# Performance work log

Measured on AMD Instinct MI355X. Metric: run time of the kernel, lower is better.

The kernel has to match this reference:

```python
import jax, jax.numpy as jnp
import numpy as np
import math

B, T, V, D, H, L = 32, 512, 16, 256, 4, 2

def _ln(x, g, b, eps=1e-5):
    m = jnp.mean(x, -1, keepdims=True)
    v = jnp.mean((x - m) ** 2, -1, keepdims=True)
    return (x - m) * jax.lax.rsqrt(v + eps) * g + b

def _grn(x, w1, b1, w2, b2, g, bn, sw=None, sb=None):
    h = jax.nn.elu(x @ w1 + b1)
    h = h @ w2 + b2
    h1, h2 = jnp.split(h, 2, axis=-1)
    h = h1 * jax.nn.sigmoid(h2)
    skip = x if sw is None else x @ sw + sb
    return _ln(h + skip, g, bn)

def setup_inputs():
    ks = iter(jax.random.split(jax.random.key(0), 64))
    s = 0.02
    def w(*shape):
        return jax.random.normal(next(ks), shape, jnp.float32) * s
    return dict(
        x=jax.random.normal(next(ks), (B, T, V), jnp.float32),
        emb_w=w(V, D), emb_b=w(V, D),
        vg_fc1_w=w(V, D, D), vg_fc1_b=w(V, D), vg_fc2_w=w(V, D, 2 * D), vg_fc2_b=w(V, 2 * D),
        vg_ln_g=jnp.ones((V, D), jnp.float32), vg_ln_b=jnp.zeros((V, D), jnp.float32),
        sel_fc1_w=w(V * D, D), sel_fc1_b=w(D), sel_fc2_w=w(D, 2 * V), sel_fc2_b=w(2 * V),
        sel_skip_w=w(V * D, V), sel_skip_b=w(V),
        sel_ln_g=jnp.ones((V,), jnp.float32), sel_ln_b=jnp.zeros((V,), jnp.float32),
        lstm_wih=w(L, 4 * D, D), lstm_whh=w(L, 4 * D, D), lstm_bih=w(L, 4 * D), lstm_bhh=w(L, 4 * D),
        pl_fc1_w=w(D, D), pl_fc1_b=w(D), pl_fc2_w=w(D, 2 * D), pl_fc2_b=w(2 * D),
        pl_ln_g=jnp.ones((D,), jnp.float32), pl_ln_b=jnp.zeros((D,), jnp.float32),
        attn_in_w=w(3 * D, D), attn_in_b=w(3 * D), attn_out_w=w(D, D), attn_out_b=w(D),
        attn_ln_g=jnp.ones((D,), jnp.float32), attn_ln_b=jnp.zeros((D,), jnp.float32),
        pa_fc1_w=w(D, D), pa_fc1_b=w(D), pa_fc2_w=w(D, 2 * D), pa_fc2_b=w(2 * D),
        pa_ln_g=jnp.ones((D,), jnp.float32), pa_ln_b=jnp.zeros((D,), jnp.float32),
        fg_fc1_w=w(D, 4 * D), fg_fc1_b=w(4 * D), fg_fc2_w=w(4 * D, 2 * D), fg_fc2_b=w(2 * D),
        fg_ln_g=jnp.ones((D,), jnp.float32), fg_ln_b=jnp.zeros((D,), jnp.float32),
    )

def reference(x, emb_w, emb_b, vg_fc1_w, vg_fc1_b, vg_fc2_w, vg_fc2_b, vg_ln_g, vg_ln_b,
              sel_fc1_w, sel_fc1_b, sel_fc2_w, sel_fc2_b, sel_skip_w, sel_skip_b, sel_ln_g, sel_ln_b,
              lstm_wih, lstm_whh, lstm_bih, lstm_bhh,
              pl_fc1_w, pl_fc1_b, pl_fc2_w, pl_fc2_b, pl_ln_g, pl_ln_b,
              attn_in_w, attn_in_b, attn_out_w, attn_out_b, attn_ln_g, attn_ln_b,
              pa_fc1_w, pa_fc1_b, pa_fc2_w, pa_fc2_b, pa_ln_g, pa_ln_b,
              fg_fc1_w, fg_fc1_b, fg_fc2_w, fg_fc2_b, fg_ln_g, fg_ln_b):
    b, t, v = x.shape
    d = emb_w.shape[1]
    # per-feature Linear(1, d) fused into one broadcasted op: [B,T,V,D]
    embedded = x[..., None] * emb_w + emb_b
    # per-variable GRNs (no skip_fc since input==output), batched over V via einsum
    h = jax.nn.elu(jnp.einsum('btvd,vdh->btvh', embedded, vg_fc1_w) + vg_fc1_b)
    h = jnp.einsum('btvh,vho->btvo', h, vg_fc2_w) + vg_fc2_b
    h1, h2 = jnp.split(h, 2, axis=-1)
    var_out = _ln(h1 * jax.nn.sigmoid(h2) + embedded, vg_ln_g, vg_ln_b)  # [B,T,V,D]
    # selection GRN over flattened variables
    flat = embedded.reshape(b, t, v * d)
    sel = _grn(flat, sel_fc1_w, sel_fc1_b, sel_fc2_w, sel_fc2_b, sel_ln_g, sel_ln_b, sel_skip_w, sel_skip_b)
    weights = jax.nn.softmax(sel, axis=-1)  # [B,T,V]
    vsn_out = jnp.einsum('btvh,btv->bth', var_out, weights)  # [B,T,D]
    # stacked LSTM (torch gate order i,f,g,o); dropout inactive at eval
    h_seq = vsn_out
    for l in range(lstm_wih.shape[0]):
        xi = jnp.einsum('btd,gd->btg', h_seq, lstm_wih[l]) + lstm_bih[l] + lstm_bhh[l]
        whh = lstm_whh[l]
        def step(carry, xt):
            hp, cp = carry
            gates = xt + hp @ whh.T
            i, f, g, o = jnp.split(gates, 4, axis=-1)
            c = jax.nn.sigmoid(f) * cp + jax.nn.sigmoid(i) * jnp.tanh(g)
            hh = jax.nn.sigmoid(o) * jnp.tanh(c)
            return (hh, c), hh
        init = (jnp.zeros((b, d), x.dtype), jnp.zeros((b, d), x.dtype))
        _, hs = jax.lax.scan(step, init, jnp.swapaxes(xi, 0, 1))
        h_seq = jnp.swapaxes(hs, 0, 1)
    lstm_filtered = _grn(h_seq + vsn_out, pl_fc1_w, pl_fc1_b, pl_fc2_w, pl_fc2_b, pl_ln_g, pl_ln_b)
    # multihead self-attention
    qkv = lstm_filtered @ attn_in_w.T + attn_in_b
    q, k, vv = jnp.split(qkv, 3, axis=-1)
    hd = d // H
    def heads(z):
        return z.reshape(b, t, H, hd).transpose(0, 2, 1, 3)
    q, k, vv = heads(q), heads(k), heads(vv)
    scale = 1.0 / math.sqrt(hd)
    att = jax.nn.softmax(jnp.einsum('bhqd,bhkd->bhqk', q, k) * scale, axis=-1)
    o = jnp.einsum('bhqk,bhkd->bhqd', att, vv).transpose(0, 2, 1, 3).reshape(b, t, d)
    o = o @ attn_out_w.T + attn_out_b
    attn_out = _ln(o + lstm_filtered, attn_ln_g, attn_ln_b)
    attn_filtered = _grn(attn_out, pa_fc1_w, pa_fc1_b, pa_fc2_w, pa_fc2_b, pa_ln_g, pa_ln_b)
    out = _grn(attn_filtered, fg_fc1_w, fg_fc1_b, fg_fc2_w, fg_fc2_b, fg_ln_g, fg_ln_b)
    return out[:, -1, :], weights
```

## Files before the change

### kernel.cpp

```cpp
#include <hip/hip_runtime.h>
#include <hip/hip_bf16.h>
#include <hip/hip_fp8.h>
#include <math.h>


#define BT 16384
#define TT 512
#define BB 32
#define VV 16
#define DD 256

typedef unsigned short ushort;
typedef unsigned int uint;
typedef unsigned long ulong_;
typedef __attribute__((ext_vector_type(8))) short short8;
typedef __attribute__((ext_vector_type(8))) unsigned short ushort8v;
typedef __attribute__((ext_vector_type(4))) float floatx4;
typedef __attribute__((ext_vector_type(8))) int int8v;

#if __has_builtin(__builtin_amdgcn_cvt_pk_fp8_f32)
#define HW_FP8_CVT 1
#endif

__device__ __forceinline__ float sigmoidf_(float x) { return 1.f / (1.f + expf(-x)); }
__device__ __forceinline__ float eluf_(float x)     { return x > 0.f ? x : expm1f(x); }
__device__ __forceinline__ float fsig(float x) {
  return __builtin_amdgcn_rcpf(1.f + __expf(-x));
}
__device__ __forceinline__ float ftanh(float x) {
  float xc = fminf(fmaxf(x, -44.f), 44.f);
  float e = __expf(-2.f * xc);
  return (1.f - e) * __builtin_amdgcn_rcpf(1.f + e);
}
__device__ __forceinline__ ushort f2bf(float f) {
  unsigned int u = __float_as_uint(f);
  unsigned int r = u + 0x7fffu + ((u >> 16) & 1u);
  return (ushort)(r >> 16);
}
__device__ __forceinline__ float bf2f(ushort b) { return __uint_as_float(((unsigned int)b) << 16); }

__device__ __forceinline__ float bsum256(float v, float* red4) {
  #pragma unroll
  for (int m = 32; m > 0; m >>= 1) v += __shfl_xor(v, m, 64);
  int w = threadIdx.x >> 6;
  if ((threadIdx.x & 63) == 0) red4[w] = v;
  __syncthreads();
  float r = red4[0] + red4[1] + red4[2] + red4[3];
  __syncthreads();
  return r;
}

__device__ __forceinline__ float block_sum256(float v, float* red) {
  int j = threadIdx.x;
  red[j] = v; __syncthreads();
  #pragma unroll
  for (int st = 128; st > 0; st >>= 1) {
    if (j < st) red[j] += red[j + st];
    __syncthreads();
  }
  float r = red[0];
  __syncthreads();
  return r;
}

__global__ void wtT_k(const float* __restrict__ src, ushort* __restrict__ dst,
                      int K, int N, long sStride, long dStride) {
  int b = blockIdx.z;
  src += (size_t)b * sStride; dst += (size_t)b * dStride;
  __shared__ float t[32][33];
  int k0 = blockIdx.y * 32, n0 = blockIdx.x * 32;
  int tx = threadIdx.x & 31, ty = threadIdx.x >> 5;
  #pragma unroll
  for (int i = 0; i < 32; i += 8) {
    int k = k0 + ty + i, n = n0 + tx;
    t[ty + i][tx] = (k < K && n < N) ? src[(size_t)k * N + n] : 0.f;
  }
  __syncthreads();
  #pragma unroll
  for (int i = 0; i < 32; i += 8) {
    int n = n0 + ty + i, k = k0 + tx;
    if (n < N && k < K) dst[(size_t)n * K + k] = f2bf(t[tx][ty + i]);
  }
}

__global__ void cvt_k(const float* __restrict__ src, ushort* __restrict__ dst, int n) {
  int i = blockIdx.x * 256 + threadIdx.x;
  if (i < n) dst[i] = f2bf(src[i]);
}

__global__ void whh_pack8_k(const float* __restrict__ whh, unsigned char* __restrict__ dst) {
  int gid = blockIdx.x * 256 + threadIdx.x;
  int layer = gid >> 13;
  int rem = gid & 8191;
  int lane = rem & 63;
  int f = (rem >> 6) & 15;
  int wave = rem >> 10;
  int kt2 = f & 1, ts = (f >> 1) & 1, g = f >> 2;
  int n = g * 256 + wave * 32 + ts * 16 + (lane & 15);
  int k0 = kt2 * 128 + (lane >> 4) * 32;
  const float* src = whh + (size_t)layer * 262144 + (size_t)n * 256 + k0;
  unsigned char* d = dst + (size_t)gid * 32;
  #pragma unroll
  for (int b = 0; b < 32; b++) {
    __hip_fp8_e4m3 q(src[b] * 64.f);
    d[b] = q.__x;
  }
}

template<int ADT, int ACT, int CDT>
__global__ __launch_bounds__(256) void mgemm_k(
    const void* __restrict__ Aall, int lda, long aStride,
    const ushort* __restrict__ Ball, long bStride,
    const float* __restrict__ biasAll, long biasStride,
    void* __restrict__ Call, int ldc, long cStride,
    int K, int Nvalid,
    const float* __restrict__ embw, const float* __restrict__ embb, int xbase) {
  int z = blockIdx.z;
  const ushort* B = Ball + (size_t)z * bStride;
  const float* bias = biasAll ? biasAll + (size_t)z * biasStride : nullptr;
  int m0 = blockIdx.y * 128, n0 = blockIdx.x * 128;
  __shared__ ushort As[128][40];
  __shared__ ushort Bs[128][40];
  int tid = threadIdx.x;
  int r = tid >> 1, half = tid & 1;
  int wave = tid >> 6, lane = tid & 63;
  int wm = (wave >> 1) * 64, wn = (wave & 1) * 64;
  int lm = lane & 15, lq = lane >> 4;
  floatx4 acc[4][4];
  #pragma unroll
  for (int i = 0; i < 4; i++)
    #pragma unroll
    for (int j = 0; j < 4; j++) acc[i][j] = (floatx4)0.f;

  for (int k0 = 0; k0 < K; k0 += 32) {
    int kk = k0 + half * 16;
    {
      int gm = m0 + r;
      ushort tmp[16];
      if (ADT == 0) {
        const float* Af = (const float*)Aall + (size_t)z * aStride + (size_t)gm * lda + kk;
        #pragma unroll
        for (int q = 0; q < 4; q++) {
          float4 f = ((const float4*)Af)[q];
          tmp[q * 4 + 0] = f2bf(f.x); tmp[q * 4 + 1] = f2bf(f.y);
          tmp[q * 4 + 2] = f2bf(f.z); tmp[q * 4 + 3] = f2bf(f.w);
        }
      } else if (ADT == 1) {
        const ushort* Ab = (const ushort*)Aall + (size_t)z * aStride + (size_t)gm * lda + kk;
        *(ushort8v*)&tmp[0] = *(const ushort8v*)(Ab);
        *(ushort8v*)&tmp[8] = *(const ushort8v*)(Ab + 8);
      } else {
        const float* xp = (const float*)Aall;
        float xv = xp[(size_t)gm * lda + xbase + z + (kk >> 8)];
        const float4* ew = (const float4*)(embw + (size_t)z * 256 + kk);
        const float4* eb = (const float4*)(embb + (size_t)z * 256 + kk);
        #pragma unroll
        for (int q = 0; q < 4; q++) {
          float4 w4 = ew[q], b4 = eb[q];
          tmp[q * 4 + 0] = f2bf(xv * w4.x + b4.x); tmp[q * 4 + 1] = f2bf(xv * w4.y + b4.y);
          tmp[q * 4 + 2] = f2bf(xv * w4.z + b4.z); tmp[q * 4 + 3] = f2bf(xv * w4.w + b4.w);
        }
      }
      *(ushort8v*)&As[r][half * 16]     = *(ushort8v*)&tmp[0];
      *(ushort8v*)&As[r][half * 16 + 8] = *(ushort8v*)&tmp[8];
    }
    {
      int gn = n0 + r;
      ushort tmp[16];
      if (gn < Nvalid) {
        const ushort* Bp = B + (size_t)gn * K + kk;
        *(ushort8v*)&tmp[0] = *(const ushort8v*)(Bp);
        *(ushort8v*)&tmp[8] = *(const ushort8v*)(Bp + 8);
      } else {
        #pragma unroll
        for (int q = 0; q < 16; q++) tmp[q] = 0;
      }
      *(ushort8v*)&Bs[r][half * 16]     = *(ushort8v*)&tmp[0];
      *(ushort8v*)&Bs[r][half * 16 + 8] = *(ushort8v*)&tmp[8];
    }
    __syncthreads();
    short8 fa[4], fb[4];
    #pragma unroll
    for (int i = 0; i < 4; i++) fa[i] = *(const short8*)&As[wm + i * 16 + lm][lq * 8];
    #pragma unroll
    for (int j = 0; j < 4; j++) fb[j] = *(const short8*)&Bs[wn + j * 16 + lm][lq * 8];
    #pragma unroll
    for (int i = 0; i < 4; i++)
      #pragma unroll
      for (int j = 0; j < 4; j++)
        acc[i][j] = __builtin_amdgcn_mfma_f32_16x16x32_bf16(fa[i], fb[j], acc[i][j], 0, 0, 0);
    __syncthreads();
  }
  #pragma unroll
  for (int j = 0; j < 4; j++) {
    int gn = n0 + wn + j * 16 + lm;
    if (gn >= Nvalid) continue;
    float bv = bias ? bias[gn] : 0.f;
    #pragma unroll
    for (int i = 0; i < 4; i++) {
      #pragma unroll
      for (int rg = 0; rg < 4; rg++) {
        int gm = m0 + wm + i * 16 + lq * 4 + rg;
        float v = acc[i][j][rg] + bv;
        if (ACT == 1) v = eluf_(v);
        if (CDT == 0) ((float*)Call + (size_t)z * cStride)[(size_t)gm * ldc + gn] = v;
        else ((ushort*)Call + (size_t)z * cStride)[(size_t)gm * ldc + gn] = f2bf(v);
      }
    }
  }
}

__global__ void sel_finish_k(const float* __restrict__ selG, const float* __restrict__ selSkip,
                             const float* __restrict__ lng, const float* __restrict__ lnb,
                             float* __restrict__ wout, int M) {
  int m = blockIdx.x * 256 + threadIdx.x;
  if (m >= M) return;
  float s[16];
  float mean = 0.f;
  #pragma unroll
  for (int i = 0; i < 16; i++) {
    float h1 = selG[m * 32 + i], h2 = selG[m * 32 + 16 + i];
    float val = h1 * sigmoidf_(h2) + selSkip[m * 16 + i];
    s[i] = val; mean += val;
  }
  mean *= (1.f / 16.f);
  float var = 0.f;
  #pragma unroll
  for (int i = 0; i < 16; i++) { float d = s[i] - mean; var += d * d; }
  var *= (1.f / 16.f);
  float inv = rsqrtf(var + 1e-5f);
  float mx = -1e30f;
  #pragma unroll
  for (int i = 0; i < 16; i++) { s[i] = (s[i] - mean) * inv * lng[i] + lnb[i]; mx = fmaxf(mx, s[i]); }
  float sum = 0.f;
  #pragma unroll
  for (int i = 0; i < 16; i++) { s[i] = expf(s[i] - mx); sum += s[i]; }
  float isum = 1.f / sum;
  #pragma unroll
  for (int i = 0; i < 16; i++) wout[m * 16 + i] = s[i] * isum;
}

__global__ __launch_bounds__(256) void var_epi4_k(
    const ushort* __restrict__ G16,
    const float* __restrict__ x, int vbase,
    const float* __restrict__ embw, const float* __restrict__ embb,
    const float* __restrict__ lng, const float* __restrict__ lnb,
    const float* __restrict__ wts, float* __restrict__ vsn, int first) {
  int m = blockIdx.x, j = threadIdx.x;
  __shared__ float red4[4];
  float accv = 0.f;
  #pragma unroll
  for (int z = 0; z < 4; z++) {
    int v = vbase + z;
    const ushort* Gp = G16 + ((size_t)z * BT + m) * 512;
    float g1 = bf2f(Gp[j]), g2 = bf2f(Gp[256 + j]);
    float e = x[m * VV + v] * embw[z * 256 + j] + embb[z * 256 + j];
    float s = g1 * sigmoidf_(g2) + e;
    float mean = bsum256(s, red4) * (1.f / 256.f);
    float d = s - mean;
    float var = bsum256(d * d, red4) * (1.f / 256.f);
    float o = d * rsqrtf(var + 1e-5f) * lng[z * 256 + j] + lnb[z * 256 + j];
    accv += wts[m * VV + v] * o;
  }
  size_t oi = (size_t)m * 256 + j;
  if (first) vsn[oi] = accv; else vsn[oi] += accv;
}

__global__ __launch_bounds__(256) void grn_epi_k(
    const ushort* __restrict__ G, const float* __restrict__ skip,
    const float* __restrict__ lng, const float* __restrict__ lnb,
    float* __restrict__ out) {
  int m = blockIdx.x, j = threadIdx.x;
  __shared__ float red4[4];
  float g1 = bf2f(G[(size_t)m * 512 + j]), g2 = bf2f(G[(size_t)m * 512 + 256 + j]);
  float s = g1 * sigmoidf_(g2) + skip[(size_t)m * 256 + j];
  float mean = bsum256(s, red4) * (1.f / 256.f);
  float d = s - mean;
  float var = bsum256(d * d, red4) * (1.f / 256.f);
  out[(size_t)m * 256 + j] = d * rsqrtf(var + 1e-5f) * lng[j] + lnb[j];
}

__global__ void add2_k(const float* __restrict__ a, const float* __restrict__ b,
                       float* __restrict__ c, int n) {
  int i = blockIdx.x * 256 + threadIdx.x;
  if (i < n) c[i] = a[i] + b[i];
}

#define DESC (1.f / 1024.f)
#define H8S 272
__global__ __launch_bounds__(512, 2) void lstm_recur_k(
    const float* __restrict__ xi,
    const unsigned char* __restrict__ wpk,
    float* __restrict__ hout,
    int T) {
  int bb = blockIdx.x;
  int tid = threadIdx.x;
  int wave = tid >> 6, lane = tid & 63;
  int lm = lane & 15, lq = lane >> 4;
  __shared__ __align__(16) unsigned char h8[2][16 * H8S];
  for (int i = tid; i < 2 * 16 * H8S / 4; i += 512) ((uint*)h8)[i] = 0;

  int8v wr[16];
  {
    const int8v* wp = (const int8v*)wpk;
    #pragma unroll
    for (int f = 0; f < 16; f++) wr[f] = wp[(wave * 16 + f) * 64 + lane];
  }
  bool act = (lq == 0);
  int jj = wave * 32 + lm;
  const float* xg = xi + (size_t)bb * T * 1024;
  float xq[8], xn[8];
  if (act) {
    #pragma unroll
    for (int g = 0; g < 4; g++) {
      xq[2 * g]     = xg[g * 256 + jj];
      xq[2 * g + 1] = xg[g * 256 + jj + 16];
    }
  }
  float cst[2] = {0.f, 0.f};
  float hbf[2][8];
  int arow = lm * H8S + lq * 32;
  __syncthreads();

  for (int t = 0; t < T; t++) {
    int cur = t & 1, nxt = cur ^ 1;
    if (act && t + 1 < T) {
      const float* xp = xg + (size_t)(t + 1) * 1024;
      #pragma unroll
      for (int g = 0; g < 4; g++) {
        xn[2 * g]     = xp[g * 256 + jj];
        xn[2 * g + 1] = xp[g * 256 + jj + 16];
      }
    }
    int8v a[2];
    #pragma unroll
    for (int kt = 0; kt < 2; kt++)
      a[kt] = *(const int8v*)&h8[cur][arow + kt * 128];
    floatx4 acc[8];
    #pragma unroll
    for (int f = 0; f < 8; f++) acc[f] = (floatx4)0.f;
    #pragma unroll
    for (int kt = 0; kt < 2; kt++)
      #pragma unroll
      for (int f = 0; f < 8; f++)
        acc[f] = __builtin_amdgcn_mfma_scale_f32_16x16x128_f8f6f4(
            a[kt], wr[f * 2 + kt], acc[f], 0, 0, 0, 0x7f7f7f7f, 0, 0x7f7f7f7f);
    if (act) {
      int tb = t & 7;
      #pragma unroll
      for (int ts = 0; ts < 2; ts++) {
        float pi = acc[0 + ts][0] * DESC + xq[0 + ts];
        float pf = acc[2 + ts][0] * DESC + xq[2 + ts];
        float pg = acc[4 + ts][0] * DESC + xq[4 + ts];
        float po = acc[6 + ts][0] * DESC + xq[6 + ts];
        float c = fsig(pf) * cst[ts] + fsig(pi) * ftanh(pg);
        cst[ts] = c;
        hbf[ts][tb] = fsig(po) * ftanh(c);
      }
#ifdef HW_FP8_CVT
      int pk = __builtin_amdgcn_cvt_pk_fp8_f32(hbf[0][tb] * 16.f, hbf[1][tb] * 16.f, 0, false);
      h8[nxt][jj]      = (unsigned char)(pk & 0xff);
      h8[nxt][jj + 16] = (unsigned char)((pk >> 8) & 0xff);
#else
      __hip_fp8_e4m3 q0(hbf[0][tb] * 16.f), q1(hbf[1][tb] * 16.f);
      h8[nxt][jj]      = q0.__x;
      h8[nxt][jj + 16] = q1.__x;
#endif
      if (tb == 7) {
        #pragma unroll
        for (int q = 0; q < 8; q++) {
          size_t base = ((size_t)(bb * T + t - 7 + q)) * 256;
          hout[base + jj]      = hbf[0][q];
          hout[base + jj + 16] = hbf[1][q];
        }
      }
      #pragma unroll
      for (int g = 0; g < 8; g++) xq[g] = xn[g];
    }
    __syncthreads();
  }
}

__global__ __launch_bounds__(256) void attn_decode_k(const float* __restrict__ qkv,
                                                     float* __restrict__ o, int T) {
  int bh = blockIdx.x; int b = bh >> 2, h = bh & 3;
  int tid = threadIdx.x;
  __shared__ float q[64];
  __shared__ float p[512];
  __shared__ float red[256];
  if (tid < 64) q[tid] = qkv[((size_t)(b * T + T - 1)) * 768 + h * 64 + tid];
  __syncthreads();
  for (int t = tid; t < 512; t += 256) {
    const float* kv = qkv + ((size_t)(b * T + t)) * 768 + 256 + h * 64;
    float s = 0.f;
    #pragma unroll 16
    for (int d = 0; d < 64; d++) s += q[d] * kv[d];
    p[t] = s * 0.125f;
  }
  __syncthreads();
  red[tid] = fmaxf(p[tid], p[tid + 256]); __syncthreads();
  for (int st = 128; st > 0; st >>= 1) { if (tid < st) red[tid] = fmaxf(red[tid], red[tid + st]); __syncthreads(); }
  float mx = red[0]; __syncthreads();
  float e0 = expf(p[tid] - mx), e1 = expf(p[tid + 256] - mx);
  red[tid] = e0 + e1; __syncthreads();
  for (int st = 128; st > 0; st >>= 1) { if (tid < st) red[tid] += red[tid + st]; __syncthreads(); }
  float inv = 1.f / red[0];
  __syncthreads();
  p[tid] = e0; p[tid + 256] = e1;
  __syncthreads();
  int d = tid & 63, grp = tid >> 6;
  float acc = 0.f;
  for (int t = grp * 128; t < grp * 128 + 128; t++)
    acc += p[t] * qkv[((size_t)(b * T + t)) * 768 + 512 + h * 64 + d];
  red[tid] = acc; __syncthreads();
  if (grp == 0)
    o[(b * 4 + h) * 64 + d] = (red[tid] + red[tid + 64] + red[tid + 128] + red[tid + 192]) * inv;
}

__global__ __launch_bounds__(256) void attn_proj_ln_k(
    const float* __restrict__ attnO, const float* __restrict__ W, const float* __restrict__ bias,
    const float* __restrict__ lstmF, const float* __restrict__ lng, const float* __restrict__ lnb,
    float* __restrict__ out, int T) {
  int bb = blockIdx.x, j = threadIdx.x;
  __shared__ float a[256];
  __shared__ float red[256];
  a[j] = attnO[bb * 256 + j];
  __syncthreads();
  float acc = bias[j];
  const float* wr = W + (size_t)j * 256;
  #pragma unroll 8
  for (int k = 0; k < 256; k += 4) {
    float4 w4 = *(const float4*)(wr + k);
    acc += a[k] * w4.x + a[k + 1] * w4.y + a[k + 2] * w4.z + a[k + 3] * w4.w;
  }
  float s = acc + lstmF[((size_t)(bb * T + T - 1)) * 256 + j];
  float mean = block_sum256(s, red) * (1.f / 256.f);
  float d = s - mean;
  float var = block_sum256(d * d, red) * (1.f / 256.f);
  out[bb * 256 + j] = d * rsqrtf(var + 1e-5f) * lng[j] + lnb[j];
}

__global__ __launch_bounds__(256) void final_grns_k(
    const float* __restrict__ ain,
    const float* __restrict__ paw1, const float* __restrict__ pab1,
    const float* __restrict__ paw2, const float* __restrict__ pab2,
    const float* __restrict__ palg, const float* __restrict__ palb,
    const float* __restrict__ fgw1, const float* __restrict__ fgb1,
    const float* __restrict__ fgw2, const float* __restrict__ fgb2,
    const float* __restrict__ fglg, const float* __restrict__ fglb,
    float* __restrict__ out) {
  int bb = blockIdx.x, j = threadIdx.x;
  __shared__ float a[256];
  __shared__ float hbuf[1024];
  __shared__ float red[256];
  a[j] = ain[bb * 256 + j];
  __syncthreads();
  float acc = pab1[j];
  for (int k = 0; k < 256; k++) acc += a[k] * paw1[k * 256 + j];
  hbuf[j] = eluf_(acc);
  __syncthreads();
  float g1 = pab2[j], g2 = pab2[256 + j];
  for (int k = 0; k < 256; k++) { float hv = hbuf[k]; g1 += hv * paw2[k * 512 + j]; g2 += hv * paw2[k * 512 + 256 + j]; }
  float s = g1 * sigmoidf_(g2) + a[j];
  float mean = block_sum256(s, red) * (1.f / 256.f);
  float d = s - mean;
  float var = block_sum256(d * d, red) * (1.f / 256.f);
  float af = d * rsqrtf(var + 1e-5f) * palg[j] + palb[j];
  __syncthreads();
  a[j] = af;
  __syncthreads();
  float hh[4];
  #pragma unroll
  for (int q = 0; q < 4; q++) {
    int jj = j + q * 256;
    float ac = fgb1[jj];
    for (int k = 0; k < 256; k++) ac += a[k] * fgw1[k * 1024 + jj];
    hh[q] = eluf_(ac);
  }
  __syncthreads();
  #pragma unroll
  for (int q = 0; q < 4; q++) hbuf[j + q * 256] = hh[q];
  __syncthreads();
  float G1 = fgb2[j], G2 = fgb2[256 + j];
  for (int k = 0; k < 1024; k++) { float hv = hbuf[k]; G1 += hv * fgw2[k * 512 + j]; G2 += hv * fgw2[k * 512 + 256 + j]; }
  float s2 = G1 * sigmoidf_(G2) + a[j];
  mean = block_sum256(s2, red) * (1.f / 256.f);
  d = s2 - mean;
  var = block_sum256(d * d, red) * (1.f / 256.f);
  out[bb * 256 + j] = d * rsqrtf(var + 1e-5f) * fglg[j] + fglb[j];
}

extern "C" void kernel_launch(void* const* d_in, const int* in_sizes, int n_in,
                              void* d_out, int out_size, void* d_ws, size_t ws_size,
                              hipStream_t stream) {
  const float* x          = (const float*)d_in[0];
  const float* emb_w      = (const float*)d_in[1];
  const float* emb_b      = (const float*)d_in[2];
  const float* vg_fc1_w   = (const float*)d_in[3];
  const float* vg_fc1_b   = (const float*)d_in[4];
  const float* vg_fc2_w   = (const float*)d_in[5];
  const float* vg_fc2_b   = (const float*)d_in[6];
  const float* vg_ln_g    = (const float*)d_in[7];
  const float* vg_ln_b    = (const float*)d_in[8];
  const float* sel_fc1_w  = (const float*)d_in[9];
  const float* sel_fc1_b  = (const float*)d_in[10];
  const float* sel_fc2_w  = (const float*)d_in[11];
  const float* sel_fc2_b  = (const float*)d_in[12];
  const float* sel_skip_w = (const float*)d_in[13];
  const float* sel_skip_b = (const float*)d_in[14];
  const float* sel_ln_g   = (const float*)d_in[15];
  const float* sel_ln_b   = (const float*)d_in[16];
  const float* lstm_wih   = (const float*)d_in[17];
  const float* lstm_whh   = (const float*)d_in[18];
  const float* lstm_bih   = (const float*)d_in[19];
  const float* lstm_bhh   = (const float*)d_in[20];
  const float* pl_fc1_w   = (const float*)d_in[21];
  const float* pl_fc1_b   = (const float*)d_in[22];
  const float* pl_fc2_w   = (const float*)d_in[23];
  const float* pl_fc2_b   = (const float*)d_in[24];
  const float* pl_ln_g    = (const float*)d_in[25];
  const float* pl_ln_b    = (const float*)d_in[26];
  const float* attn_in_w  = (const float*)d_in[27];
  const float* attn_in_b  = (const float*)d_in[28];
  const float* attn_out_w = (const float*)d_in[29];
  const float* attn_out_b = (const float*)d_in[30];
  const float* attn_ln_g  = (const float*)d_in[31];
  const float* attn_ln_b  = (const float*)d_in[32];
  const float* pa_fc1_w   = (const float*)d_in[33];
  const float* pa_fc1_b   = (const float*)d_in[34];
  const float* pa_fc2_w   = (const float*)d_in[35];
  const float* pa_fc2_b   = (const float*)d_in[36];
  const float* pa_ln_g    = (const float*)d_in[37];
  const float* pa_ln_b    = (const float*)d_in[38];
  const float* fg_fc1_w   = (const float*)d_in[39];
  const float* fg_fc1_b   = (const float*)d_in[40];
  const float* fg_fc2_w   = (const float*)d_in[41];
  const float* fg_fc2_b   = (const float*)d_in[42];
  const float* fg_ln_g    = (const float*)d_in[43];
  const float* fg_ln_b    = (const float*)d_in[44];
  (void)in_sizes; (void)n_in; (void)out_size; (void)ws_size;

  float* out     = (float*)d_out;
  float* out_wts = out + BB * DD;

  char* p = (char*)d_ws;
  ushort* wt_sel_fc1  = (ushort*)p;                 p += 1048576 * 2;
  ushort* wt_sel_skip = (ushort*)p;                 p += 65536 * 2;
  ushort* wt_sel_fc2  = (ushort*)p;                 p += 8192 * 2;
  ushort* wt_var_fc1  = (ushort*)p;                 p += 1048576 * 2;
  ushort* wt_var_fc2  = (ushort*)p;                 p += 2097152 * 2;
  ushort* wt_wih      = (ushort*)p;                 p += 524288 * 2;
  unsigned char* wt_whh_pk8 = (unsigned char*)p;    p += 524288;
  ushort* wt_pl_fc1   = (ushort*)p;                 p += 65536 * 2;
  ushort* wt_pl_fc2   = (ushort*)p;                 p += 131072 * 2;
  ushort* wt_attn     = (ushort*)p;                 p += 196608 * 2;
  ushort* selH        = (ushort*)p;                 p += (size_t)BT * 256 * 2;
  float*  selSkip     = (float*)p;                  p += (size_t)BT * 16 * 4;
  float*  selG        = (float*)p;                  p += (size_t)BT * 32 * 4;
  float*  vsn         = (float*)p;                  p += (size_t)BT * 256 * 4;
  float*  hseq1       = (float*)p;                  p += (size_t)BT * 256 * 4;
  float*  hseq2       = (float*)p;                  p += (size_t)BT * 256 * 4;
  float*  cbias       = (float*)p;                  p += 4096 * 4;
  float*  attnO       = (float*)p;                  p += 8192 * 4;
  float*  attnLN      = (float*)p;                  p += 8192 * 4;
  char*   R           = p;
  ushort* bufA16 = (ushort*)R;
  ushort* bufG16 = (ushort*)(R + (((size_t)32) << 20));
  float*  xi     = (float*)R;
  float*  plA    = (float*)R;
  ushort* plH    = (ushort*)(R + (((size_t)16) << 20));
  ushort* plG    = (ushort*)(R + (((size_t)24) << 20));
  float*  lstmF  = (float*)(R + (((size_t)48) << 20));
  float*  qkv    = (float*)R;

  dim3 blk(256);

  wtT_k<<<dim3(8, 128, 1),  blk, 0, stream>>>(sel_fc1_w,  wt_sel_fc1,  4096, 256, 0, 0);
  wtT_k<<<dim3(1, 128, 1),  blk, 0, stream>>>(sel_skip_w, wt_sel_skip, 4096, 16,  0, 0);
  wtT_k<<<dim3(1, 8, 1),    blk, 0, stream>>>(sel_fc2_w,  wt_sel_fc2,  256,  32,  0, 0);
  wtT_k<<<dim3(8, 8, 16),   blk, 0, stream>>>(vg_fc1_w,   wt_var_fc1,  256,  256, 65536, 65536);
  wtT_k<<<dim3(16, 8, 16),  blk, 0, stream>>>(vg_fc2_w,   wt_var_fc2,  256,  512, 131072, 131072);
  wtT_k<<<dim3(8, 8, 1),    blk, 0, stream>>>(pl_fc1_w,   wt_pl_fc1,   256,  256, 0, 0);
  wtT_k<<<dim3(16, 8, 1),   blk, 0, stream>>>(pl_fc2_w,   wt_pl_fc2,   256,  512, 0, 0);
  cvt_k<<<2048, blk, 0, stream>>>(lstm_wih,  wt_wih, 524288);
  whh_pack8_k<<<64, blk, 0, stream>>>(lstm_whh, wt_whh_pk8);
  cvt_k<<<768,  blk, 0, stream>>>(attn_in_w, wt_attn, 196608);
  add2_k<<<8, blk, 0, stream>>>(lstm_bih, lstm_bhh, cbias, 4096);

  mgemm_k<2,1,1><<<dim3(2, 128, 1), blk, 0, stream>>>(x, 16, 0, wt_sel_fc1, 0, sel_fc1_b, 0,
      selH, 256, 0, 4096, 256, emb_w, emb_b, 0);
  mgemm_k<2,0,0><<<dim3(1, 128, 1), blk, 0, stream>>>(x, 16, 0, wt_sel_skip, 0, sel_skip_b, 0,
      selSkip, 16, 0, 4096, 16, emb_w, emb_b, 0);
  mgemm_k<1,0,0><<<dim3(1, 128, 1), blk, 0, stream>>>(selH, 256, 0, wt_sel_fc2, 0, sel_fc2_b, 0,
      selG, 32, 0, 256, 32, nullptr, nullptr, 0);
  sel_finish_k<<<64, blk, 0, stream>>>(selG, selSkip, sel_ln_g, sel_ln_b, out_wts, BT);

  for (int g = 0; g < 4; g++) {
    mgemm_k<2,1,1><<<dim3(2, 128, 4), blk, 0, stream>>>(x, 16, 0,
        wt_var_fc1 + (size_t)g * 4 * 65536, 65536, vg_fc1_b + g * 1024, 256,
        bufA16, 256, (long)BT * 256, 256, 256, emb_w + g * 1024, emb_b + g * 1024, g * 4);
    mgemm_k<1,0,1><<<dim3(4, 128, 4), blk, 0, stream>>>(bufA16, 256, (long)BT * 256,
        wt_var_fc2 + (size_t)g * 4 * 131072, 131072, vg_fc2_b + g * 2048, 512,
        bufG16, 512, (long)BT * 512, 256, 512, nullptr, nullptr, 0);
    var_epi4_k<<<BT, blk, 0, stream>>>(bufG16, x, g * 4, emb_w + g * 1024, emb_b + g * 1024,
        vg_ln_g + g * 1024, vg_ln_b + g * 1024, out_wts, vsn, g == 0 ? 1 : 0);
  }

  mgemm_k<0,0,0><<<dim3(8, 128, 1), blk, 0, stream>>>(vsn, 256, 0, wt_wih, 0, cbias, 0,
      xi, 1024, 0, 256, 1024, nullptr, nullptr, 0);
  lstm_recur_k<<<32, 512, 0, stream>>>(xi, wt_whh_pk8, hseq1, TT);
  mgemm_k<0,0,0><<<dim3(8, 128, 1), blk, 0, stream>>>(hseq1, 256, 0, wt_wih + 1024 * 256, 0,
      cbias + 1024, 0, xi, 1024, 0, 256, 1024, nullptr, nullptr, 0);
  lstm_recur_k<<<32, 512, 0, stream>>>(xi, wt_whh_pk8 + 262144, hseq2, TT);

  add2_k<<<BT, blk, 0, stream>>>(hseq2, vsn, plA, BT * 256);
  mgemm_k<0,1,1><<<dim3(2, 128, 1), blk, 0, stream>>>(plA, 256, 0, wt_pl_fc1, 0, pl_fc1_b, 0,
      plH, 256, 0, 256, 256, nullptr, nullptr, 0);
  mgemm_k<1,0,1><<<dim3(4, 128, 1), blk, 0, stream>>>(plH, 256, 0, wt_pl_fc2, 0, pl_fc2_b, 0,
      plG, 512, 0, 256, 512, nullptr, nullptr, 0);
  grn_epi_k<<<BT, blk, 0, stream>>>(plG, plA, pl_ln_g, pl_ln_b, lstmF);

  mgemm_k<0,0,0><<<dim3(6, 128, 1), blk, 0, stream>>>(lstmF, 256, 0, wt_attn, 0, attn_in_b, 0,
      qkv, 768, 0, 256, 768, nullptr, nullptr, 0);
  attn_decode_k<<<BB * 4, blk, 0, stream>>>(qkv, attnO, TT);
  attn_proj_ln_k<<<BB, blk, 0, stream>>>(attnO, attn_out_w, attn_out_b, lstmF,
                                         attn_ln_g, attn_ln_b, attnLN, TT);

  final_grns_k<<<BB, blk, 0, stream>>>(attnLN,
      pa_fc1_w, pa_fc1_b, pa_fc2_w, pa_fc2_b, pa_ln_g, pa_ln_b,
      fg_fc1_w, fg_fc1_b, fg_fc2_w, fg_fc2_b, fg_ln_g, fg_ln_b,
      out);
}
```

Before: 2.469 ms.

## Store LSTM input projections in bf16, fuse residual add, single-pass layernorm

The LSTM input-projection GEMMs now write bf16 instead of fp32, which halves the buffer the recurrent kernel streams each step. The separate hseq2+vsn add kernel is removed: the add is folded into the pl_fc1 GEMM A-load (new ADT 3 path) and into the GRN epilogue skip. Layernorm epilogues compute sum and sum of squares in one fused reduction, cutting barriers from four to two. The first MFMA in the recurrence takes a zero accumulator directly instead of zero-initialising acc. The risks are bf16 rounding of the gate preactivations and the less stable E[x^2]-mean^2 variance formula.

```diff
diff --git a/kernel.cpp b/kernel.cpp
--- a/kernel.cpp
+++ b/kernel.cpp
@@ -39,15 +39,16 @@
 }
 __device__ __forceinline__ float bf2f(ushort b) { return __uint_as_float(((unsigned int)b) << 16); }
 
-__device__ __forceinline__ float bsum256(float v, float* red4) {
-  #pragma unroll
-  for (int m = 32; m > 0; m >>= 1) v += __shfl_xor(v, m, 64);
+__device__ __forceinline__ float2 bsum256x2(float a, float b, float* red8) {
+  #pragma unroll
+  for (int m = 32; m > 0; m >>= 1) { a += __shfl_xor(a, m, 64); b += __shfl_xor(b, m, 64); }
   int w = threadIdx.x >> 6;
-  if ((threadIdx.x & 63) == 0) red4[w] = v;
-  __syncthreads();
-  float r = red4[0] + red4[1] + red4[2] + red4[3];
-  __syncthreads();
-  return r;
+  if ((threadIdx.x & 63) == 0) { red8[w * 2] = a; red8[w * 2 + 1] = b; }
+  __syncthreads();
+  float ra = red8[0] + red8[2] + red8[4] + red8[6];
+  float rb = red8[1] + red8[3] + red8[5] + red8[7];
+  __syncthreads();
+  return make_float2(ra, rb);
 }
 
 __device__ __forceinline__ float block_sum256(float v, float* red) {
@@ -149,7 +150,7 @@
         const ushort* Ab = (const ushort*)Aall + (size_t)z * aStride + (size_t)gm * lda + kk;
         *(ushort8v*)&tmp[0] = *(const ushort8v*)(Ab);
         *(ushort8v*)&tmp[8] = *(const ushort8v*)(Ab + 8);
-      } else {
+      } else if (ADT == 2) {
         const float* xp = (const float*)Aall;
         float xv = xp[(size_t)gm * lda + xbase + z + (kk >> 8)];
         const float4* ew = (const float4*)(embw + (size_t)z * 256 + kk);
@@ -159,6 +160,16 @@
           float4 w4 = ew[q], b4 = eb[q];
           tmp[q * 4 + 0] = f2bf(xv * w4.x + b4.x); tmp[q * 4 + 1] = f2bf(xv * w4.y + b4.y);
           tmp[q * 4 + 2] = f2bf(xv * w4.z + b4.z); tmp[q * 4 + 3] = f2bf(xv * w4.w + b4.w);
+        }
+      } else {
+        const float* A1 = (const float*)Aall + (size_t)z * aStride + (size_t)gm * lda + kk;
+        const float* A2 = embw + (size_t)z * aStride + (size_t)gm * lda + kk;
+        #pragma unroll
+        for (int q = 0; q < 4; q++) {
+          float4 f1 = ((const float4*)A1)[q];
+          float4 f2 = ((const float4*)A2)[q];
+          tmp[q * 4 + 0] = f2bf(f1.x + f2.x); tmp[q * 4 + 1] = f2bf(f1.y + f2.y);
+          tmp[q * 4 + 2] = f2bf(f1.z + f2.z); tmp[q * 4 + 3] = f2bf(f1.w + f2.w);
         }
       }
       *(ushort8v*)&As[r][half * 16]     = *(ushort8v*)&tmp[0];
@@ -247,7 +258,7 @@
     const float* __restrict__ lng, const float* __restrict__ lnb,
     const float* __restrict__ wts, float* __restrict__ vsn, int first) {
   int m = blockIdx.x, j = threadIdx.x;
-  __shared__ float red4[4];
+  __shared__ float red8[8];
   float accv = 0.f;
   #pragma unroll
   for (int z = 0; z < 4; z++) {
@@ -256,10 +267,10 @@
     float g1 = bf2f(Gp[j]), g2 = bf2f(Gp[256 + j]);
     float e = x[m * VV + v] * embw[z * 256 + j] + embb[z * 256 + j];
     float s = g1 * sigmoidf_(g2) + e;
-    float mean = bsum256(s, red4) * (1.f / 256.f);
-    float d = s - mean;
-    float var = bsum256(d * d, red4) * (1.f / 256.f);
-    float o = d * rsqrtf(var + 1e-5f) * lng[z * 256 + j] + lnb[z * 256 + j];
+    float2 r = bsum256x2(s, s * s, red8);
+    float mean = r.x * (1.f / 256.f);
+    float var = r.y * (1.f / 256.f) - mean * mean;
+    float o = (s - mean) * rsqrtf(var + 1e-5f) * lng[z * 256 + j] + lnb[z * 256 + j];
     accv += wts[m * VV + v] * o;
   }
   size_t oi = (size_t)m * 256 + j;
@@ -267,17 +278,20 @@
 }
 
 __global__ __launch_bounds__(256) void grn_epi_k(
-    const ushort* __restrict__ G, const float* __restrict__ skip,
+    const ushort* __restrict__ G, const float* __restrict__ skipA,
+    const float* __restrict__ skipB,
     const float* __restrict__ lng, const float* __restrict__ lnb,
     float* __restrict__ out) {
   int m = blockIdx.x, j = threadIdx.x;
-  __shared__ float red4[4];
+  __shared__ float red8[8];
   float g1 = bf2f(G[(size_t)m * 512 + j]), g2 = bf2f(G[(size_t)m * 512 + 256 + j]);
-  float s = g1 * sigmoidf_(g2) + skip[(size_t)m * 256 + j];
-  float mean = bsum256(s, red4) * (1.f / 256.f);
-  float d = s - mean;
-  float var = bsum256(d * d, red4) * (1.f / 256.f);
-  out[(size_t)m * 256 + j] = d * rsqrtf(var + 1e-5f) * lng[j] + lnb[j];
+  float sk = skipA[(size_t)m * 256 + j];
+  if (skipB) sk += skipB[(size_t)m * 256 + j];
+  float s = g1 * sigmoidf_(g2) + sk;
+  float2 r = bsum256x2(s, s * s, red8);
+  float mean = r.x * (1.f / 256.f);
+  float var = r.y * (1.f / 256.f) - mean * mean;
+  out[(size_t)m * 256 + j] = (s - mean) * rsqrtf(var + 1e-5f) * lng[j] + lnb[j];
 }
 
 __global__ void add2_k(const float* __restrict__ a, const float* __restrict__ b,
@@ -289,7 +303,7 @@
 #define DESC (1.f / 1024.f)
 #define H8S 272
 __global__ __launch_bounds__(512, 2) void lstm_recur_k(
-    const float* __restrict__ xi,
+    const ushort* __restrict__ xi16,
     const unsigned char* __restrict__ wpk,
     float* __restrict__ hout,
     int T) {
@@ -308,28 +322,29 @@
   }
   bool act = (lq == 0);
   int jj = wave * 32 + lm;
-  const float* xg = xi + (size_t)bb * T * 1024;
+  const ushort* xg = xi16 + (size_t)bb * T * 1024;
   float xq[8], xn[8];
   if (act) {
     #pragma unroll
     for (int g = 0; g < 4; g++) {
-      xq[2 * g]     = xg[g * 256 + jj];
-      xq[2 * g + 1] = xg[g * 256 + jj + 16];
+      xq[2 * g]     = bf2f(xg[g * 256 + jj]);
+      xq[2 * g + 1] = bf2f(xg[g * 256 + jj + 16]);
     }
   }
   float cst[2] = {0.f, 0.f};
   float hbf[2][8];
   int arow = lm * H8S + lq * 32;
+  const floatx4 z4 = (floatx4)0.f;
   __syncthreads();
 
   for (int t = 0; t < T; t++) {
     int cur = t & 1, nxt = cur ^ 1;
     if (act && t + 1 < T) {
-      const float* xp = xg + (size_t)(t + 1) * 1024;
+      const ushort* xp = xg + (size_t)(t + 1) * 1024;
       #pragma unroll
       for (int g = 0; g < 4; g++) {
-        xn[2 * g]     = xp[g * 256 + jj];
-        xn[2 * g + 1] = xp[g * 256 + jj + 16];
+        xn[2 * g]     = bf2f(xp[g * 256 + jj]);
+        xn[2 * g + 1] = bf2f(xp[g * 256 + jj + 16]);
       }
     }
     int8v a[2];
@@ -338,13 +353,13 @@
       a[kt] = *(const int8v*)&h8[cur][arow + kt * 128];
     floatx4 acc[8];
     #pragma unroll
-    for (int f = 0; f < 8; f++) acc[f] = (floatx4)0.f;
-    #pragma unroll
-    for (int kt = 0; kt < 2; kt++)
-      #pragma unroll
-      for (int f = 0; f < 8; f++)
-        acc[f] = __builtin_amdgcn_mfma_scale_f32_16x16x128_f8f6f4(
-            a[kt], wr[f * 2 + kt], acc[f], 0, 0, 0, 0x7f7f7f7f, 0, 0x7f7f7f7f);
+    for (int f = 0; f < 8; f++)
+      acc[f] = __builtin_amdgcn_mfma_scale_f32_16x16x128_f8f6f4(
+          a[0], wr[f * 2 + 0], z4, 0, 0, 0, 0x7f7f7f7f, 0, 0x7f7f7f7f);
+    #pragma unroll
+    for (int f = 0; f < 8; f++)
+      acc[f] = __builtin_amdgcn_mfma_scale_f32_16x16x128_f8f6f4(
+          a[1], wr[f * 2 + 1], acc[f], 0, 0, 0, 0x7f7f7f7f, 0, 0x7f7f7f7f);
     if (act) {
       int tb = t & 7;
       #pragma unroll
@@ -566,8 +581,7 @@
   char*   R           = p;
   ushort* bufA16 = (ushort*)R;
   ushort* bufG16 = (ushort*)(R + (((size_t)32) << 20));
-  float*  xi     = (float*)R;
-  float*  plA    = (float*)R;
+  ushort* xi16   = (ushort*)R;
   ushort* plH    = (ushort*)(R + (((size_t)16) << 20));
   ushort* plG    = (ushort*)(R + (((size_t)24) << 20));
   float*  lstmF  = (float*)(R + (((size_t)48) << 20));
@@ -606,19 +620,18 @@
         vg_ln_g + g * 1024, vg_ln_b + g * 1024, out_wts, vsn, g == 0 ? 1 : 0);
   }
 
-  mgemm_k<0,0,0><<<dim3(8, 128, 1), blk, 0, stream>>>(vsn, 256, 0, wt_wih, 0, cbias, 0,
-      xi, 1024, 0, 256, 1024, nullptr, nullptr, 0);
-  lstm_recur_k<<<32, 512, 0, stream>>>(xi, wt_whh_pk8, hseq1, TT);
-  mgemm_k<0,0,0><<<dim3(8, 128, 1), blk, 0, stream>>>(hseq1, 256, 0, wt_wih + 1024 * 256, 0,
-      cbias + 1024, 0, xi, 1024, 0, 256, 1024, nullptr, nullptr, 0);
-  lstm_recur_k<<<32, 512, 0, stream>>>(xi, wt_whh_pk8 + 262144, hseq2, TT);
-
-  add2_k<<<BT, blk, 0, stream>>>(hseq2, vsn, plA, BT * 256);
-  mgemm_k<0,1,1><<<dim3(2, 128, 1), blk, 0, stream>>>(plA, 256, 0, wt_pl_fc1, 0, pl_fc1_b, 0,
-      plH, 256, 0, 256, 256, nullptr, nullptr, 0);
+  mgemm_k<0,0,1><<<dim3(8, 128, 1), blk, 0, stream>>>(vsn, 256, 0, wt_wih, 0, cbias, 0,
+      xi16, 1024, 0, 256, 1024, nullptr, nullptr, 0);
+  lstm_recur_k<<<32, 512, 0, stream>>>(xi16, wt_whh_pk8, hseq1, TT);
+  mgemm_k<0,0,1><<<dim3(8, 128, 1), blk, 0, stream>>>(hseq1, 256, 0, wt_wih + 1024 * 256, 0,
+      cbias + 1024, 0, xi16, 1024, 0, 256, 1024, nullptr, nullptr, 0);
+  lstm_recur_k<<<32, 512, 0, stream>>>(xi16, wt_whh_pk8 + 262144, hseq2, TT);
+
+  mgemm_k<3,1,1><<<dim3(2, 128, 1), blk, 0, stream>>>(hseq2, 256, 0, wt_pl_fc1, 0, pl_fc1_b, 0,
+      plH, 256, 0, 256, 256, vsn, nullptr, 0);
   mgemm_k<1,0,1><<<dim3(4, 128, 1), blk, 0, stream>>>(plH, 256, 0, wt_pl_fc2, 0, pl_fc2_b, 0,
       plG, 512, 0, 256, 512, nullptr, nullptr, 0);
-  grn_epi_k<<<BT, blk, 0, stream>>>(plG, plA, pl_ln_g, pl_ln_b, lstmF);
+  grn_epi_k<<<BT, blk, 0, stream>>>(plG, hseq2, vsn, pl_ln_g, pl_ln_b, lstmF);
 
   mgemm_k<0,0,0><<<dim3(6, 128, 1), blk, 0, stream>>>(lstmF, 256, 0, wt_attn, 0, attn_in_b, 0,
       qkv, 768, 0, 256, 768, nullptr, nullptr, 0);
```

Measured after the change: 2.542 ms. 3.0% more time.
